# Performance work log

Measured on AMD Instinct MI355X. Metric: run time of the kernel, lower is better.

## Reference

```python
import jax, jax.numpy as jnp
import numpy as np

STRIDES = (4, 8, 16, 32, 64)
RATIOS = (0.5, 1.0, 2.0)
SCALE = 8.0
A = 3
PRE_NMS = 2000
MAX_PER_IMG = 1000
NMS_THR = 0.7
MAX_RATIO = float(abs(np.log(16.0 / 1000.0)))  # wh_ratio_clip = 16/1000
LEVEL_OFFSET = 4096.0  # > max image coordinate, separates levels for batched NMS
FEAT_HW = ((208, 336), (104, 168), (52, 84), (26, 42), (13, 21))
N = 8


def grid_anchors(stride, H, W):
    # mmdet-style base anchors: scale 8, ratios (0.5,1,2), centered at 0
    r = jnp.asarray(RATIOS, jnp.float32)
    h_r = jnp.sqrt(r)
    w_r = 1.0 / h_r
    ws = stride * w_r * SCALE
    hs = stride * h_r * SCALE
    base = jnp.stack([-ws / 2, -hs / 2, ws / 2, hs / 2], axis=-1)  # [A,4]
    sx = jnp.arange(W, dtype=jnp.float32) * stride
    sy = jnp.arange(H, dtype=jnp.float32) * stride
    yy, xx = jnp.meshgrid(sy, sx, indexing='ij')
    shifts = jnp.stack([xx, yy, xx, yy], axis=-1).reshape(-1, 4)  # [H*W,4], row-major
    return (shifts[:, None, :] + base[None, :, :]).reshape(-1, 4)  # [H*W*A,4]


def decode(anchors, deltas, h, w):
    # DeltaXYWH decode with means 0, stds 1, clip to image
    px = (anchors[..., 0] + anchors[..., 2]) * 0.5
    py = (anchors[..., 1] + anchors[..., 3]) * 0.5
    pw = anchors[..., 2] - anchors[..., 0]
    ph = anchors[..., 3] - anchors[..., 1]
    dx, dy = deltas[..., 0], deltas[..., 1]
    dw = jnp.clip(deltas[..., 2], -MAX_RATIO, MAX_RATIO)
    dh = jnp.clip(deltas[..., 3], -MAX_RATIO, MAX_RATIO)
    gx = px + pw * dx
    gy = py + ph * dy
    gw = pw * jnp.exp(dw)
    gh = ph * jnp.exp(dh)
    x1 = jnp.clip(gx - gw * 0.5, 0.0, w)
    y1 = jnp.clip(gy - gh * 0.5, 0.0, h)
    x2 = jnp.clip(gx + gw * 0.5, 0.0, w)
    y2 = jnp.clip(gy + gh * 0.5, 0.0, h)
    return jnp.stack([x1, y1, x2, y2], axis=-1)


def iou_matrix(b):
    area = (b[:, 2] - b[:, 0]) * (b[:, 3] - b[:, 1])
    lt = jnp.maximum(b[:, None, :2], b[None, :, :2])
    rb = jnp.minimum(b[:, None, 2:], b[None, :, 2:])
    wh = jnp.clip(rb - lt, 0.0, None)
    inter = wh[..., 0] * wh[..., 1]
    union = area[:, None] + area[None, :] - inter
    return inter / jnp.maximum(union, 1e-6)


def _forward(cls_list, reg_list, image_h, image_w):
    scores_all, deltas_all, anchors_all, levels_all = [], [], [], []
    for lvl, (cls, reg) in enumerate(zip(cls_list, reg_list)):
        n, _, H, W = cls.shape
        anchors = grid_anchors(STRIDES[lvl], H, W)  # [H*W*A,4]
        s = jax.nn.sigmoid(jnp.transpose(cls, (0, 2, 3, 1)).reshape(n, -1))
        d = jnp.transpose(reg, (0, 2, 3, 1)).reshape(n, -1, 4)
        k = min(PRE_NMS, s.shape[1])  # topk pre-selection per level
        sv, si = jax.lax.top_k(s, k)
        dv = jnp.take_along_axis(d, si[..., None], axis=1)
        av = anchors[si]
        scores_all.append(sv)
        deltas_all.append(dv)
        anchors_all.append(av)
        levels_all.append(jnp.full((k,), lvl, jnp.int32))
    scores = jnp.concatenate(scores_all, axis=1)    # [N,M]
    deltas = jnp.concatenate(deltas_all, axis=1)    # [N,M,4]
    anchors = jnp.concatenate(anchors_all, axis=1)  # [N,M,4]
    levels = jnp.concatenate(levels_all)            # [M] (same per image)
    boxes = decode(anchors, deltas, float(image_h), float(image_w))
    # filter_boxes with min_area = prod((0,0)) = 0: keep boxes with area >= 0
    area = (boxes[..., 2] - boxes[..., 0]) * (boxes[..., 3] - boxes[..., 1])
    scores = jnp.where(area >= 0.0, scores, -1.0)
    M = boxes.shape[1]
    idxs = jnp.arange(M)

    def nms_one(bs):
        b_i, s_i = bs
        order = jnp.argsort(-s_i)
        b = b_i[order]
        s = s_i[order]
        lv = levels[order]
        # batched NMS: offset each level so cross-level boxes never overlap
        ob = jax.lax.stop_gradient(b + (lv.astype(b.dtype) * LEVEL_OFFSET)[:, None])
        iou = iou_matrix(ob)  # [M,M]

        def body(i, keep):
            sup = (iou[i] > NMS_THR) & (idxs > i) & keep[i]
            return keep & (~sup)

        keep = jax.lax.fori_loop(0, M, body, jnp.ones((M,), bool))
        rank = jnp.cumsum(keep.astype(jnp.int32)) - 1
        tgt = jnp.where(keep & (rank < MAX_PER_IMG), rank, MAX_PER_IMG)  # dump slot
        out_b = jnp.zeros((MAX_PER_IMG + 1, 4), b.dtype).at[tgt].set(b)[:MAX_PER_IMG]
        out_s = jnp.zeros((MAX_PER_IMG + 1,), s.dtype).at[tgt].set(s)[:MAX_PER_IMG]
        return out_b, out_s

    pb, ps = jax.lax.map(nms_one, (boxes, scores))  # sequential per image
    return pb, ps  # [N,1000,4], [N,1000] (zero-padded)


def setup_inputs() -> dict:
    key = jax.random.key(0)
    inp = {}
    for lvl, (H, W) in enumerate(FEAT_HW):
        k1 = jax.random.fold_in(key, 2 * lvl)
        k2 = jax.random.fold_in(key, 2 * lvl + 1)
        inp[f"class_out_{lvl}"] = jax.random.normal(k1, (N, A, H, W), jnp.float32)
        inp[f"reg_out_{lvl}"] = jax.random.normal(k2, (N, 4 * A, H, W), jnp.float32)
    inp["image_h"] = 832
    inp["image_w"] = 1344
    return inp


def reference(class_out_0, class_out_1, class_out_2, class_out_3, class_out_4,
              reg_out_0, reg_out_1, reg_out_2, reg_out_3, reg_out_4,
              image_h, image_w):
    cls_list = [class_out_0, class_out_1, class_out_2, class_out_3, class_out_4]
    reg_list = [reg_out_0, reg_out_1, reg_out_2, reg_out_3, reg_out_4]
    return _forward(cls_list, reg_list, image_h, image_w)
```

## Files before the change

kernel.cpp:

```cpp
#include <hip/hip_runtime.h>
#include <cmath>

#pragma clang fp contract(off)

namespace {
constexpr int NIMG = 8;
constexpr int NLVL = 5;
constexpr int LH[5]   = {208,104,52,26,13};
constexpr int LW[5]   = {336,168,84,42,21};
constexpr int LSTR[5] = {4,8,16,32,64};
constexpr int HWA[5]  = {209664,52416,13104,3276,819};
constexpr int KSEL[5] = {2000,2000,2000,2000,819};
constexpr int SOFF[5] = {0,2000,4000,6000,8000};
constexpr int MTOT    = 8819;
constexpr int CAP     = 6144;
constexpr int NPAIR   = NIMG*NLVL;
constexpr int CCUM[5] = {52,65,69,70,71};
constexpr int BLK_PER_IMG = 71;
constexpr int MASK_W  = 32;
constexpr int OUTK    = 1000;

constexpr size_t OFF_HIST   = 0;
constexpr size_t OFF_PKC    = 0;
constexpr size_t OFF_CNT    = 655360;
constexpr size_t OFF_THR    = 655520;
constexpr size_t ZERO_BYTES = 655680;
constexpr size_t OFF_CAND   = 655872;
constexpr size_t OFF_SELIDX = 1638912;
constexpr size_t OFF_SELKEY = 1921120;
constexpr size_t OFF_SELSC  = 2485536;
constexpr size_t OFF_SELBOX = 2767744;
constexpr size_t OFF_MASK   = 3896576;
constexpr size_t OFF_CKEY   = OFF_MASK;
constexpr size_t OFF_KEEP   = 24376576;
}

struct Ins {
  const float* cls[5];
  const float* reg[5];
  const int* ih;
  const int* iw;
};

__device__ __forceinline__ void decode_block(int b, int& img, int& lvl, int& chunk) {
  img = b / BLK_PER_IMG;
  int rb = b - img*BLK_PER_IMG;
  if      (rb < CCUM[0]) { lvl=0; chunk=rb; }
  else if (rb < CCUM[1]) { lvl=1; chunk=rb-CCUM[0]; }
  else if (rb < CCUM[2]) { lvl=2; chunk=rb-CCUM[1]; }
  else if (rb < CCUM[3]) { lvl=3; chunk=rb-CCUM[2]; }
  else                   { lvl=4; chunk=0; }
}

__device__ __forceinline__ unsigned mapbits(float x) {
  unsigned u = __float_as_uint(x);
  return u ^ (unsigned)(((int)u >> 31) | (int)0x80000000);
}

__device__ __forceinline__ float sigmoid_ref(float x) {
  float e = (float)exp(-(double)x);
  return 1.0f / (1.0f + e);
}

__global__ void k_hist(Ins in, unsigned* __restrict__ hist) {
  int img, lvl, chunk; decode_block(blockIdx.x, img, lvl, chunk);
  __shared__ unsigned lh[4096];
  for (int i = threadIdx.x; i < 4096; i += 256) lh[i] = 0;
  __syncthreads();
  const float* src = in.cls[lvl] + (size_t)img * HWA[lvl];
  if (lvl != 4) {
    const float4* src4 = (const float4*)src;
    int nf4 = HWA[lvl] >> 2;
    int base4 = chunk * 1024;
    #pragma unroll
    for (int j = 0; j < 4; j++) {
      int f = base4 + j*256 + threadIdx.x;
      if (f < nf4) {
        float4 v = src4[f];
        atomicAdd(&lh[mapbits(v.x) >> 20], 1u);
        atomicAdd(&lh[mapbits(v.y) >> 20], 1u);
        atomicAdd(&lh[mapbits(v.z) >> 20], 1u);
        atomicAdd(&lh[mapbits(v.w) >> 20], 1u);
      }
    }
  } else {
    int base = chunk * 4096;
    #pragma unroll
    for (int j = 0; j < 16; j++) {
      int e = base + j*256 + threadIdx.x;
      if (e < HWA[4]) atomicAdd(&lh[mapbits(src[e]) >> 20], 1u);
    }
  }
  __syncthreads();
  unsigned* gh = hist + (img*NLVL + lvl) * 4096;
  for (int i = threadIdx.x; i < 4096; i += 256)
    if (lh[i]) atomicAdd(&gh[i], lh[i]);
}

__global__ void k_scan(const unsigned* __restrict__ hist, unsigned* __restrict__ thr) {
  int pair = blockIdx.x; int lvl = pair % NLVL;
  const unsigned* h = hist + (size_t)pair * 4096;
  __shared__ unsigned part[256];
  unsigned s = 0;
  #pragma unroll
  for (int i = 0; i < 16; i++) s += h[threadIdx.x*16 + i];
  part[threadIdx.x] = s;
  __syncthreads();
  if (threadIdx.x == 0) {
    unsigned k = (unsigned)KSEL[lvl];
    unsigned cum = 0;
    unsigned edge = 0;
    for (int t = 255; t >= 0; t--) {
      if (cum + part[t] >= k) {
        for (int b = t*16 + 15; b >= t*16; b--) {
          cum += h[b];
          if (cum >= k) { edge = (unsigned)b; break; }
        }
        thr[pair] = edge << 20;
        return;
      }
      cum += part[t];
    }
    thr[pair] = 0u;
  }
}

__global__ void __launch_bounds__(256) k_compact(Ins in, const unsigned* __restrict__ thr,
                          unsigned* __restrict__ cnt, unsigned* __restrict__ cand,
                          unsigned long long* __restrict__ ckey) {
  int img, lvl, chunk; decode_block(blockIdx.x, img, lvl, chunk);
  int pair = img*NLVL + lvl;
  unsigned T = thr[pair];
  const float* src = in.cls[lvl] + (size_t)img * HWA[lvl];
  int hw = LH[lvl] * LW[lvl];
  int lid = threadIdx.x & 63;
  __shared__ unsigned lbuf[4096];
  __shared__ unsigned long long lkey[4096];
  __shared__ unsigned lc, gbase;
  if (threadIdx.x == 0) lc = 0;
  __syncthreads();

  auto emit = [&](int e, float v, bool sel) {
    unsigned long long mask = __ballot(sel);
    if (mask != 0ull) {
      int leader = __ffsll((long long)mask) - 1;
      unsigned wb = 0;
      if (lid == leader) wb = atomicAdd(&lc, (unsigned)__popcll(mask));
      wb = (unsigned)__shfl((int)wb, leader, 64);
      if (sel) {
        unsigned p = wb + (unsigned)__popcll(mask & ((1ull << lid) - 1ull));
        int a = e / hw;
        int r = e - a*hw;
        unsigned idx = (unsigned)(r*3 + a);
        lbuf[p] = idx;
        float s = sigmoid_ref(v);
        unsigned pack = ((unsigned)lvl << 18) | idx;
        lkey[p] = ((unsigned long long)__float_as_uint(s) << 21)
                | (unsigned long long)(0x1FFFFFu - pack);
      }
    }
  };

  if (lvl != 4) {
    const float4* src4 = (const float4*)src;
    int nf4 = HWA[lvl] >> 2;
    int base4 = chunk * 1024;
    #pragma unroll
    for (int j = 0; j < 4; j++) {
      int f = base4 + j*256 + threadIdx.x;
      bool inb = f < nf4;
      float4 v4 = make_float4(0.f, 0.f, 0.f, 0.f);
      if (inb) v4 = src4[f];
      int e0 = f * 4;
      emit(e0+0, v4.x, inb && (mapbits(v4.x) >= T));
      emit(e0+1, v4.y, inb && (mapbits(v4.y) >= T));
      emit(e0+2, v4.z, inb && (mapbits(v4.z) >= T));
      emit(e0+3, v4.w, inb && (mapbits(v4.w) >= T));
    }
  } else {
    int base = chunk * 4096;
    #pragma unroll
    for (int j = 0; j < 16; j++) {
      int e = base + j*256 + threadIdx.x;
      float v = 0.0f;
      bool inb = (e < HWA[4]);
      if (inb) v = src[e];
      emit(e, v, inb && (mapbits(v) >= T));
    }
  }
  __syncthreads();
  if (threadIdx.x == 0) gbase = atomicAdd(&cnt[pair], lc);
  __syncthreads();
  unsigned nsel = lc, gb = gbase;
  for (unsigned t = threadIdx.x; t < nsel; t += 256) {
    unsigned p = gb + t;
    if (p < CAP) {
      cand[(size_t)pair*CAP + p] = lbuf[t];
      ckey[(size_t)pair*CAP + p] = lkey[t];
    }
  }
}

__global__ void __launch_bounds__(256) k_rank(Ins in, const unsigned* __restrict__ cntA,
                       const unsigned* __restrict__ cand,
                       const unsigned long long* __restrict__ ckey,
                       unsigned long long* __restrict__ sel_key,
                       float* __restrict__ sel_sc,
                       float* __restrict__ sel_box) {
  int pair = blockIdx.y; int tile = blockIdx.x;
  int img = pair / NLVL, lvl = pair % NLVL;
  int c = min((int)cntA[pair], CAP);
  if (tile*256 >= c) return;
  __shared__ unsigned long long keys[CAP];
  const unsigned long long* kp = ckey + (size_t)pair*CAP;
  for (int j = threadIdx.x; j < c; j += 256) keys[j] = kp[j];
  __syncthreads();
  int jj = tile*256 + threadIdx.x;
  if (jj >= c) return;
  unsigned long long mykey = keys[jj];
  int rk = 0;
  for (int j = 0; j < c; j++) rk += (keys[j] > mykey) ? 1 : 0;
  if (rk < KSEL[lvl]) {
    int slot = img*MTOT + SOFF[lvl] + rk;
    sel_key[slot] = mykey;
    sel_sc[slot]  = __uint_as_float((unsigned)(mykey >> 21));
    unsigned idx = cand[(size_t)pair*CAP + jj];
    int a = (int)(idx % 3u);
    int r = (int)(idx / 3u);
    int Wl = LW[lvl]; int hw = LH[lvl]*Wl;
    int x = r % Wl, y = r / Wl;
    const float* rg = in.reg[lvl] + (size_t)img * 4 * HWA[lvl];
    float dx = rg[(a*4+0)*hw + r];
    float dy = rg[(a*4+1)*hw + r];
    float dw = rg[(a*4+2)*hw + r];
    float dh = rg[(a*4+3)*hw + r];
    float ratio = (a==0) ? 0.5f : (a==1) ? 1.0f : 2.0f;
    float hr = sqrtf(ratio);
    float wr = 1.0f / hr;
    float st = (float)LSTR[lvl];
    float wsz = st * wr * 8.0f;
    float hsz = st * hr * 8.0f;
    float xs = (float)x * st, ys = (float)y * st;
    float x1 = xs - wsz*0.5f, x2 = xs + wsz*0.5f;
    float y1 = ys - hsz*0.5f, y2 = ys + hsz*0.5f;
    float px = (x1 + x2) * 0.5f, py = (y1 + y2) * 0.5f;
    float pw = x2 - x1,          ph = y2 - y1;
    const float MR = 4.135166556742356f;
    dw = fminf(fmaxf(dw, -MR), MR);
    dh = fminf(fmaxf(dh, -MR), MR);
    float gx = px + pw*dx, gy = py + ph*dy;
    float gw = pw * (float)exp((double)dw);
    float gh = ph * (float)exp((double)dh);
    float Wi = (float)(*in.iw), Hi = (float)(*in.ih);
    float4 bb;
    bb.x = fminf(fmaxf(gx - gw*0.5f, 0.0f), Wi);
    bb.y = fminf(fmaxf(gy - gh*0.5f, 0.0f), Hi);
    bb.z = fminf(fmaxf(gx + gw*0.5f, 0.0f), Wi);
    bb.w = fminf(fmaxf(gy + gh*0.5f, 0.0f), Hi);
    ((float4*)sel_box)[slot] = bb;
  }
}

__global__ void __launch_bounds__(256) k_masks(const float* __restrict__ sel_box,
                        unsigned long long* __restrict__ maskbuf) {
  int pair = blockIdx.y; int lvl = pair % NLVL; int img = pair / NLVL;
  int n = KSEL[lvl];
  int nw = (n + 63) >> 6;
  int wv = threadIdx.x >> 6;
  int lane = threadIdx.x & 63;
  int t = blockIdx.x * 4 + wv;
  int ntile = nw * (nw + 1) / 2;
  if (t >= ntile) return;
  int rb = 0, cum = 0;
  while (cum + (nw - rb) <= t) { cum += nw - rb; rb++; }
  int jw = rb + (t - cum);
  const float4* boxes = ((const float4*)sel_box) + img*MTOT + SOFF[lvl];
  float off = (float)lvl * 4096.0f;
  int col = jw*64 + lane;
  float bjx, bjy, bjz, bjw2, aj;
  if (col < n) {
    float4 bj = boxes[col];
    bjx = bj.x + off; bjy = bj.y + off; bjz = bj.z + off; bjw2 = bj.w + off;
    aj = (bjz - bjx) * (bjw2 - bjy);
  } else {
    bjx = 3.0e8f; bjy = 3.0e8f; bjz = 3.0e8f; bjw2 = 3.0e8f;
    aj = 0.0f;
  }
  __shared__ float4 srow[4][64];
  int row0 = rb*64;
  {
    float4 bi0 = boxes[min(row0 + lane, n-1)];
    bi0.x += off; bi0.y += off; bi0.z += off; bi0.w += off;
    srow[wv][lane] = bi0;
  }
  const double Md = 0.70000001788139343261718750;
  unsigned long long acc = 0ull;
  if (jw > rb) {
    #pragma unroll 16
    for (int r = 0; r < 64; r++) {
      float4 bi = srow[wv][r];
      float ai = (bi.z - bi.x) * (bi.w - bi.y);
      float xx1 = fmaxf(bi.x, bjx), yy1 = fmaxf(bi.y, bjy);
      float xx2 = fminf(bi.z, bjz), yy2 = fminf(bi.w, bjw2);
      float iw_ = fmaxf(xx2 - xx1, 0.0f), ih_ = fmaxf(yy2 - yy1, 0.0f);
      float inter = iw_ * ih_;
      float u = fmaxf((ai + aj) - inter, 1e-6f);
      bool sup = (double)inter >= Md * (double)u;
      unsigned long long word = __ballot(sup);
      if (lane == r) acc = word;
    }
  } else {
    #pragma unroll 16
    for (int r = 0; r < 64; r++) {
      float4 bi = srow[wv][r];
      float ai = (bi.z - bi.x) * (bi.w - bi.y);
      float xx1 = fmaxf(bi.x, bjx), yy1 = fmaxf(bi.y, bjy);
      float xx2 = fminf(bi.z, bjz), yy2 = fminf(bi.w, bjw2);
      float iw_ = fmaxf(xx2 - xx1, 0.0f), ih_ = fmaxf(yy2 - yy1, 0.0f);
      float inter = iw_ * ih_;
      float u = fmaxf((ai + aj) - inter, 1e-6f);
      bool sup = (double)inter >= Md * (double)u;
      unsigned long long word = __ballot(sup) & ~((2ull << r) - 1ull);
      if (lane == r) acc = word;
    }
  }
  if (row0 + lane < n)
    maskbuf[(size_t)pair*2000*MASK_W + (size_t)(row0 + lane)*MASK_W + jw] = acc;
}

__global__ void __launch_bounds__(1024) k_nms(const unsigned long long* __restrict__ maskbuf,
                      unsigned long long* __restrict__ keep, int* __restrict__ pkc) {
  int pair = blockIdx.x; int lvl = pair % NLVL;
  int n = KSEL[lvl];
  int nw = (n + 63) >> 6;
  const unsigned long long* mrow = maskbuf + (size_t)pair*2000*MASK_W;
  int tid = threadIdx.x;
  int w  = tid & 31;
  int rg = tid >> 5;
  __shared__ unsigned long long rem[32];
  __shared__ unsigned long long diag[64];
  __shared__ unsigned long long skw[32];
  __shared__ unsigned long long sSk;
  __shared__ int lcnt[64];
  if (tid < 32) { rem[tid] = 0ull; skw[tid] = 0ull; }
  __syncthreads();

  unsigned long long A0, A1, B0, B1;
  {
    int r0 = min(rg*2, n-1), r1 = min(rg*2+1, n-1);
    A0 = mrow[(size_t)r0*MASK_W + w];
    A1 = mrow[(size_t)r1*MASK_W + w];
  }
  for (int k = 0; k < nw; k++) {
    if (k + 1 < nw) {
      int r0 = min(64*(k+1) + rg*2, n-1), r1 = min(64*(k+1) + rg*2 + 1, n-1);
      B0 = mrow[(size_t)r0*MASK_W + w];
      B1 = mrow[(size_t)r1*MASK_W + w];
    }
    if (w == k) { diag[rg*2] = A0; diag[rg*2+1] = A1; }
    __syncthreads();
    if (tid < 64) {
      int row = 64*k + tid;
      bool valid = row < n;
      unsigned long long D = valid ? diag[tid] : 0ull;
      unsigned long long rk = rem[k];
      unsigned long long S = rk;
      for (int it = 0; it < 64; it++) {
        bool kept = valid && !((S >> tid) & 1ull);
        unsigned long long c = kept ? D : 0ull;
        #pragma unroll
        for (int m = 1; m < 64; m <<= 1) {
          unsigned lo = (unsigned)__shfl_xor((int)(unsigned)(c & 0xffffffffull), m, 64);
          unsigned hi = (unsigned)__shfl_xor((int)(unsigned)(c >> 32), m, 64);
          c |= ((unsigned long long)hi << 32) | (unsigned long long)lo;
        }
        unsigned long long Snew = rk | c;
        if (Snew == S) break;
        S = Snew;
      }
      if (tid == 0) {
        sSk = S;
        int nb = n - 64*k;
        unsigned long long vm = (nb >= 64) ? ~0ull : ((1ull << nb) - 1ull);
        unsigned long long kw = (~S) & vm;
        skw[k] = kw;
        keep[(size_t)pair*MASK_W + k] = kw;
      }
    }
    __syncthreads();
    if (w > k) {
      unsigned long long Sk = sSk;
      int r0 = 64*k + rg*2, r1 = r0 + 1;
      unsigned long long m = 0ull;
      if (r0 < n && !((Sk >> (rg*2)) & 1ull))     m |= A0;
      if (r1 < n && !((Sk >> (rg*2+1)) & 1ull))   m |= A1;
      if (m) atomicOr(&rem[w], m);
    }
    __syncthreads();
    A0 = B0; A1 = B1;
  }
  if (tid < 64) {
    int lane = tid;
    unsigned long long kw = (lane < nw) ? skw[lane] : 0ull;
    lcnt[lane] = __popcll(kw);
    int pre = 0;
    for (int t2 = 0; t2 < lane; t2++) pre += lcnt[t2];
    for (int b = 0; b < 64; b++) {
      int p = lane*64 + b;
      if (p < n) {
        pre += (int)((kw >> b) & 1ull);
        pkc[pair*2048 + p] = pre;
      }
    }
  }
}

__global__ void __launch_bounds__(256) k_out2(const unsigned long long* __restrict__ sel_key,
                      const float* __restrict__ sel_box,
                      const unsigned long long* __restrict__ keep,
                      const int* __restrict__ pkc,
                      float* __restrict__ out) {
  int img = blockIdx.y;
  int pos = blockIdx.x*256 + threadIdx.x;
  if (pos >= MTOT) return;
  int lvl = pos<2000?0 : pos<4000?1 : pos<6000?2 : pos<8000?3 : 4;
  int local = pos - SOFF[lvl];
  int pair = img*NLVL + lvl;
  unsigned long long kw = keep[(size_t)pair*MASK_W + (local >> 6)];
  if (!((kw >> (local & 63)) & 1ull)) return;
  unsigned long long mykey = sel_key[img*MTOT + pos];
  int rank = pkc[pair*2048 + local] - 1;
  #pragma unroll
  for (int l2 = 0; l2 < NLVL; l2++) {
    if (l2 == lvl) continue;
    const unsigned long long* A = sel_key + img*MTOT + SOFF[l2];
    int lo = 0, hi = KSEL[l2];
    while (lo < hi) {
      int mid = (lo + hi) >> 1;
      if (A[mid] > mykey) lo = mid + 1; else hi = mid;
    }
    if (lo > 0) rank += pkc[(img*NLVL + l2)*2048 + lo - 1];
  }
  if (rank < OUTK) {
    ((float4*)out)[img*OUTK + rank] = ((const float4*)sel_box)[img*MTOT + pos];
    out[NIMG*OUTK*4 + img*OUTK + rank] = __uint_as_float((unsigned)(mykey >> 21));
  }
}

extern "C" void kernel_launch(void* const* d_in, const int* in_sizes, int n_in,
                              void* d_out, int out_size, void* d_ws, size_t ws_size,
                              hipStream_t stream) {
  Ins in;
  for (int l = 0; l < 5; l++) {
    in.cls[l] = (const float*)d_in[2*l];
    in.reg[l] = (const float*)d_in[2*l + 1];
  }
  in.ih = (const int*)d_in[10];
  in.iw = (const int*)d_in[11];

  char* ws = (char*)d_ws;
  unsigned* hist              = (unsigned*)(ws + OFF_HIST);
  int* pkc                    = (int*)(ws + OFF_PKC);
  unsigned* cnt               = (unsigned*)(ws + OFF_CNT);
  unsigned* thr               = (unsigned*)(ws + OFF_THR);
  unsigned* cand              = (unsigned*)(ws + OFF_CAND);
  unsigned long long* sel_key = (unsigned long long*)(ws + OFF_SELKEY);
  float* sel_sc               = (float*)(ws + OFF_SELSC);
  float* sel_box              = (float*)(ws + OFF_SELBOX);
  unsigned long long* maskbuf = (unsigned long long*)(ws + OFF_MASK);
  unsigned long long* ckey    = (unsigned long long*)(ws + OFF_CKEY);
  unsigned long long* keep    = (unsigned long long*)(ws + OFF_KEEP);
  float* out                  = (float*)d_out;

  hipMemsetAsync(d_ws, 0, ZERO_BYTES, stream);
  hipMemsetAsync(d_out, 0, (size_t)NIMG*OUTK*5*sizeof(float), stream);

  k_hist   <<<NIMG*BLK_PER_IMG, 256, 0, stream>>>(in, hist);
  k_scan   <<<NPAIR, 256, 0, stream>>>(hist, thr);
  k_compact<<<NIMG*BLK_PER_IMG, 256, 0, stream>>>(in, thr, cnt, cand, ckey);
  k_rank   <<<dim3(CAP/256, NPAIR), 256, 0, stream>>>(in, cnt, cand, ckey, sel_key, sel_sc, sel_box);
  k_masks  <<<dim3(132, NPAIR), 256, 0, stream>>>(sel_box, maskbuf);
  k_nms    <<<NPAIR, 1024, 0, stream>>>(maskbuf, keep, pkc);
  k_out2   <<<dim3((MTOT + 255)/256, NIMG), 256, 0, stream>>>(sel_key, sel_box, keep, pkc, out);
}
```

Before: 277.4 us.

## Rank keys via wave ballots and process two mask columns per wave with float fast path

New measurement: 268.8 us. 3.1% less time.

```diff
diff --git a/kernel.cpp b/kernel.cpp
--- a/kernel.cpp
+++ b/kernel.cpp
@@ -19,6 +19,7 @@
 constexpr int BLK_PER_IMG = 71;
 constexpr int MASK_W  = 32;
 constexpr int OUTK    = 1000;
+constexpr int NT2[5]  = {272,272,272,272,55};
 
 constexpr size_t OFF_HIST   = 0;
 constexpr size_t OFF_PKC    = 0;
@@ -26,7 +27,6 @@
 constexpr size_t OFF_THR    = 655520;
 constexpr size_t ZERO_BYTES = 655680;
 constexpr size_t OFF_CAND   = 655872;
-constexpr size_t OFF_SELIDX = 1638912;
 constexpr size_t OFF_SELKEY = 1921120;
 constexpr size_t OFF_SELSC  = 2485536;
 constexpr size_t OFF_SELBOX = 2767744;
@@ -211,16 +211,40 @@
   int img = pair / NLVL, lvl = pair % NLVL;
   int c = min((int)cntA[pair], CAP);
   if (tile*256 >= c) return;
-  __shared__ unsigned long long keys[CAP];
   const unsigned long long* kp = ckey + (size_t)pair*CAP;
-  for (int j = threadIdx.x; j < c; j += 256) keys[j] = kp[j];
-  __syncthreads();
   int jj = tile*256 + threadIdx.x;
-  if (jj >= c) return;
-  unsigned long long mykey = keys[jj];
+  bool act = jj < c;
+  unsigned long long mykey = kp[min(jj, c-1)];
+  int lane = threadIdx.x & 63;
   int rk = 0;
-  for (int j = 0; j < c; j++) rk += (keys[j] > mykey) ? 1 : 0;
-  if (rk < KSEL[lvl]) {
+
+  auto window = [&](int w0, bool tail) {
+    const ulonglong2* kp2 = (const ulonglong2*)(kp + w0);
+    ulonglong2 A = kp2[lane];
+    ulonglong2 B = kp2[64 + lane];
+    if (tail) {
+      int i = w0 + 2*lane;
+      if (i     >= c) A.x = 0ull;
+      if (i + 1 >= c) A.y = 0ull;
+      if (i + 128 >= c) B.x = 0ull;
+      if (i + 129 >= c) B.y = 0ull;
+    }
+    #pragma unroll
+    for (int mk = 0; mk < 64; mk++) {
+      unsigned mlo = (unsigned)__builtin_amdgcn_readlane((int)(unsigned)mykey, mk);
+      unsigned mhi = (unsigned)__builtin_amdgcn_readlane((int)(unsigned)(mykey >> 32), mk);
+      unsigned long long smk = ((unsigned long long)mhi << 32) | (unsigned long long)mlo;
+      int add = __popcll(__ballot(A.x > smk)) + __popcll(__ballot(A.y > smk))
+              + __popcll(__ballot(B.x > smk)) + __popcll(__ballot(B.y > smk));
+      if (lane == mk) rk += add;
+    }
+  };
+
+  int nfull = c >> 8;
+  for (int w = 0; w < nfull; w++) window(w*256, false);
+  if (c & 255) window(nfull*256, true);
+
+  if (act && rk < KSEL[lvl]) {
     int slot = img*MTOT + SOFF[lvl] + rk;
     sel_key[slot] = mykey;
     sel_sc[slot]  = __uint_as_float((unsigned)(mykey >> 21));
@@ -266,66 +290,102 @@
   int pair = blockIdx.y; int lvl = pair % NLVL; int img = pair / NLVL;
   int n = KSEL[lvl];
   int nw = (n + 63) >> 6;
+  int nwc2 = (nw + 1) >> 1;
   int wv = threadIdx.x >> 6;
   int lane = threadIdx.x & 63;
   int t = blockIdx.x * 4 + wv;
-  int ntile = nw * (nw + 1) / 2;
-  if (t >= ntile) return;
+  if (t >= NT2[lvl]) return;
   int rb = 0, cum = 0;
-  while (cum + (nw - rb) <= t) { cum += nw - rb; rb++; }
-  int jw = rb + (t - cum);
+  while (cum + (nwc2 - (rb >> 1)) <= t) { cum += nwc2 - (rb >> 1); rb++; }
+  int jw2 = (rb >> 1) + (t - cum);
+  int jw0 = 2*jw2, jw1 = jw0 + 1;
   const float4* boxes = ((const float4*)sel_box) + img*MTOT + SOFF[lvl];
   float off = (float)lvl * 4096.0f;
-  int col = jw*64 + lane;
-  float bjx, bjy, bjz, bjw2, aj;
-  if (col < n) {
-    float4 bj = boxes[col];
-    bjx = bj.x + off; bjy = bj.y + off; bjz = bj.z + off; bjw2 = bj.w + off;
-    aj = (bjz - bjx) * (bjw2 - bjy);
-  } else {
-    bjx = 3.0e8f; bjy = 3.0e8f; bjz = 3.0e8f; bjw2 = 3.0e8f;
-    aj = 0.0f;
-  }
-  __shared__ float4 srow[4][64];
+  int c0 = jw0*64 + lane, c1 = c0 + 64;
+  float b0x,b0y,b0z,b0w,a0, b1x,b1y,b1z,b1w,a1;
+  if (c0 < n) {
+    float4 b = boxes[c0];
+    b0x = b.x + off; b0y = b.y + off; b0z = b.z + off; b0w = b.w + off;
+    a0 = (b0z - b0x) * (b0w - b0y);
+  } else { b0x=b0y=b0z=b0w=3.0e8f; a0=0.0f; }
+  if (c1 < n) {
+    float4 b = boxes[c1];
+    b1x = b.x + off; b1y = b.y + off; b1z = b.z + off; b1w = b.w + off;
+    a1 = (b1z - b1x) * (b1w - b1y);
+  } else { b1x=b1y=b1z=b1w=3.0e8f; a1=0.0f; }
+  __shared__ float4 sbox[4][64];
+  __shared__ float  sarea[4][64];
   int row0 = rb*64;
   {
     float4 bi0 = boxes[min(row0 + lane, n-1)];
     bi0.x += off; bi0.y += off; bi0.z += off; bi0.w += off;
-    srow[wv][lane] = bi0;
-  }
-  const double Md = 0.70000001788139343261718750;
-  unsigned long long acc = 0ull;
-  if (jw > rb) {
-    #pragma unroll 16
+    sbox[wv][lane] = bi0;
+    sarea[wv][lane] = (bi0.z - bi0.x) * (bi0.w - bi0.y);
+  }
+  bool z0 = (jw0 < rb);
+  bool d0 = (jw0 == rb), d1 = (jw1 == rb);
+  const float CHI = 0x1.66666ap-1f;
+  const float CLO = 0x1.666664p-1f;
+  unsigned long long acc0 = 0ull, acc1 = 0ull, unc = 0ull;
+  #pragma unroll 16
+  for (int r = 0; r < 64; r++) {
+    float4 bi = sbox[wv][r];
+    float ai = sarea[wv][r];
+    float xx1 = fmaxf(bi.x, b0x), yy1 = fmaxf(bi.y, b0y);
+    float xx2 = fminf(bi.z, b0z), yy2 = fminf(bi.w, b0w);
+    float iw_ = fmaxf(xx2 - xx1, 0.0f), ih_ = fmaxf(yy2 - yy1, 0.0f);
+    float in0 = iw_ * ih_;
+    float u0 = fmaxf((ai + a0) - in0, 1e-6f);
+    float xc1 = fmaxf(bi.x, b1x), yc1 = fmaxf(bi.y, b1y);
+    float xc2 = fminf(bi.z, b1z), yc2 = fminf(bi.w, b1w);
+    float jw_ = fmaxf(xc2 - xc1, 0.0f), jh_ = fmaxf(yc2 - yc1, 0.0f);
+    float in1 = jw_ * jh_;
+    float u1 = fmaxf((ai + a1) - in1, 1e-6f);
+    unsigned long long h0 = __ballot(in0 >= CHI * u0);
+    unsigned long long l0 = __ballot(in0 >= CLO * u0);
+    unsigned long long h1 = __ballot(in1 >= CHI * u1);
+    unsigned long long l1 = __ballot(in1 >= CLO * u1);
+    unc |= (h0 ^ l0) | (h1 ^ l1);
+    unsigned long long dm = ~((2ull << r) - 1ull);
+    unsigned long long m0 = z0 ? 0ull : (d0 ? (h0 & dm) : h0);
+    unsigned long long m1 = d1 ? (h1 & dm) : h1;
+    if (lane == r) { acc0 = m0; acc1 = m1; }
+  }
+  if (unc) {
+    const double Md = 0.70000001788139343261718750;
+    acc0 = 0ull; acc1 = 0ull;
+    #pragma unroll 1
     for (int r = 0; r < 64; r++) {
-      float4 bi = srow[wv][r];
-      float ai = (bi.z - bi.x) * (bi.w - bi.y);
-      float xx1 = fmaxf(bi.x, bjx), yy1 = fmaxf(bi.y, bjy);
-      float xx2 = fminf(bi.z, bjz), yy2 = fminf(bi.w, bjw2);
+      float4 bi = sbox[wv][r];
+      float ai = sarea[wv][r];
+      float xx1 = fmaxf(bi.x, b0x), yy1 = fmaxf(bi.y, b0y);
+      float xx2 = fminf(bi.z, b0z), yy2 = fminf(bi.w, b0w);
       float iw_ = fmaxf(xx2 - xx1, 0.0f), ih_ = fmaxf(yy2 - yy1, 0.0f);
-      float inter = iw_ * ih_;
-      float u = fmaxf((ai + aj) - inter, 1e-6f);
-      bool sup = (double)inter >= Md * (double)u;
-      unsigned long long word = __ballot(sup);
-      if (lane == r) acc = word;
-    }
-  } else {
-    #pragma unroll 16
-    for (int r = 0; r < 64; r++) {
-      float4 bi = srow[wv][r];
-      float ai = (bi.z - bi.x) * (bi.w - bi.y);
-      float xx1 = fmaxf(bi.x, bjx), yy1 = fmaxf(bi.y, bjy);
-      float xx2 = fminf(bi.z, bjz), yy2 = fminf(bi.w, bjw2);
-      float iw_ = fmaxf(xx2 - xx1, 0.0f), ih_ = fmaxf(yy2 - yy1, 0.0f);
-      float inter = iw_ * ih_;
-      float u = fmaxf((ai + aj) - inter, 1e-6f);
-      bool sup = (double)inter >= Md * (double)u;
-      unsigned long long word = __ballot(sup) & ~((2ull << r) - 1ull);
-      if (lane == r) acc = word;
-    }
-  }
-  if (row0 + lane < n)
-    maskbuf[(size_t)pair*2000*MASK_W + (size_t)(row0 + lane)*MASK_W + jw] = acc;
+      float in0 = iw_ * ih_;
+      float u0 = fmaxf((ai + a0) - in0, 1e-6f);
+      float xc1 = fmaxf(bi.x, b1x), yc1 = fmaxf(bi.y, b1y);
+      float xc2 = fminf(bi.z, b1z), yc2 = fminf(bi.w, b1w);
+      float jw_ = fmaxf(xc2 - xc1, 0.0f), jh_ = fmaxf(yc2 - yc1, 0.0f);
+      float in1 = jw_ * jh_;
+      float u1 = fmaxf((ai + a1) - in1, 1e-6f);
+      unsigned long long w0 = __ballot((double)in0 >= Md * (double)u0);
+      unsigned long long w1 = __ballot((double)in1 >= Md * (double)u1);
+      unsigned long long dm = ~((2ull << r) - 1ull);
+      unsigned long long m0 = z0 ? 0ull : (d0 ? (w0 & dm) : w0);
+      unsigned long long m1 = d1 ? (w1 & dm) : w1;
+      if (lane == r) { acc0 = m0; acc1 = m1; }
+    }
+  }
+  int row = row0 + lane;
+  if (row < n) {
+    unsigned long long* dst = maskbuf + (size_t)pair*2000*MASK_W + (size_t)row*MASK_W + jw0;
+    if (z0) {
+      dst[1] = acc1;
+    } else {
+      ulonglong2 v; v.x = acc0; v.y = acc1;
+      *((ulonglong2*)dst) = v;
+    }
+  }
 }
 
 __global__ void __launch_bounds__(1024) k_nms(const unsigned long long* __restrict__ maskbuf,
@@ -479,7 +539,7 @@
   k_scan   <<<NPAIR, 256, 0, stream>>>(hist, thr);
   k_compact<<<NIMG*BLK_PER_IMG, 256, 0, stream>>>(in, thr, cnt, cand, ckey);
   k_rank   <<<dim3(CAP/256, NPAIR), 256, 0, stream>>>(in, cnt, cand, ckey, sel_key, sel_sc, sel_box);
-  k_masks  <<<dim3(132, NPAIR), 256, 0, stream>>>(sel_box, maskbuf);
+  k_masks  <<<dim3(68, NPAIR), 256, 0, stream>>>(sel_box, maskbuf);
   k_nms    <<<NPAIR, 1024, 0, stream>>>(maskbuf, keep, pkc);
   k_out2   <<<dim3((MTOT + 255)/256, NIMG), 256, 0, stream>>>(sel_key, sel_box, keep, pkc, out);
 }
```
